# Kernel tuning notes

Hardware: AMD Instinct MI355X
Metric: run time of the kernel (lower is better)

Reference implementation:

```python
import jax, jax.numpy as jnp
import numpy as np

N_NODES = 50000
N_EDGES = 800000
D = 128


def _gcn_layer(x, src, dst, deg_inv_sqrt, W, b, n_nodes):
    # GCNConv: X' = D^{-1/2} (A + I) D^{-1/2} X W + b   (PyG default, self-loops added)
    h = x @ W  # [N, D]
    norm = deg_inv_sqrt[src] * deg_inv_sqrt[dst]  # [E+N]
    msgs = h[src] * norm[:, None]  # [E+N, D] gather + scale
    out = jax.ops.segment_sum(msgs, dst, num_segments=n_nodes)  # scatter-add
    return out + b


def setup_inputs() -> dict:
    key = jax.random.key(0)
    k1, k2, k3, k4 = jax.random.split(key, 4)
    x = jax.random.normal(k1, (N_NODES, D), dtype=jnp.float32)
    edge_index = jax.random.randint(k2, (2, N_EDGES), 0, N_NODES, dtype=jnp.int64)
    scale = 1.0 / np.sqrt(D)
    W1 = jax.random.normal(k3, (D, D), dtype=jnp.float32) * scale
    b1 = jnp.zeros((D,), dtype=jnp.float32)
    W2 = jax.random.normal(k4, (D, D), dtype=jnp.float32) * scale
    b2 = jnp.zeros((D,), dtype=jnp.float32)
    return {"x": x, "edge_index": edge_index, "W1": W1, "b1": b1, "W2": W2, "b2": b2}


def reference(x, edge_index, W1, b1, W2, b2):
    n_nodes = x.shape[0]
    # add self-loops once (same graph both layers)
    loop = jnp.arange(n_nodes, dtype=edge_index.dtype)
    src = jnp.concatenate([edge_index[0], loop])
    dst = jnp.concatenate([edge_index[1], loop])
    deg = jax.ops.segment_sum(jnp.ones_like(dst, dtype=x.dtype), dst, num_segments=n_nodes)
    deg_inv_sqrt = jnp.where(deg > 0, jax.lax.rsqrt(deg), 0.0)

    h = _gcn_layer(x, src, dst, deg_inv_sqrt, W1, b1, n_nodes)
    h = jax.nn.relu(h)
    h = _gcn_layer(h, src, dst, deg_inv_sqrt, W2, b2, n_nodes)
    h = jax.nn.relu(h)
    return h
```

## Files before the change

kernel.cpp:

```cpp
#include <hip/hip_runtime.h>

#define N_NODES 50000
#define N_EDGES 800000
#define D 128
#define NB 196
#define CHUNK 4096
#define NBKT 196
#define LHM (NBKT * NB)
#define NSB 151

typedef unsigned int uint32;
typedef unsigned short ushort;
typedef __attribute__((ext_vector_type(8))) short s8v;
typedef __attribute__((ext_vector_type(4))) float f4v;

__device__ __forceinline__ ushort f2bf(float f) {
    unsigned u = __float_as_uint(f);
    u += 0x7FFFu + ((u >> 16) & 1u);
    return (ushort)(u >> 16);
}
__device__ __forceinline__ float bf_lo(uint32 u) { return __uint_as_float(u << 16); }
__device__ __forceinline__ float bf_hi(uint32 u) { return __uint_as_float(u & 0xFFFF0000u); }

__device__ __forceinline__ int block_incl_scan(int v, int t) {
    int lane = t & 63, wv = t >> 6;
    int incl = v;
    #pragma unroll
    for (int off = 1; off < 64; off <<= 1) {
        int u = __shfl_up(incl, off, 64);
        if (lane >= off) incl += u;
    }
    __shared__ int wsums[4];
    if (lane == 63) wsums[wv] = incl;
    __syncthreads();
    int add = 0;
    if (wv > 0) add += wsums[0];
    if (wv > 1) add += wsums[1];
    if (wv > 2) add += wsums[2];
    return incl + add;
}

__global__ __launch_bounds__(256) void phaseA_kernel(const int* __restrict__ dst,
                                                     int* __restrict__ histM) {
    __shared__ int cnt[NBKT];
    int t = threadIdx.x, blk = blockIdx.x;
    if (t < NBKT) cnt[t] = 0;
    __syncthreads();
    int e0 = blk * CHUNK;
    for (int i = t; i < CHUNK; i += 256) {
        int e = e0 + i;
        if (e < N_EDGES) atomicAdd(&cnt[dst[e] >> 8], 1);
    }
    __syncthreads();
    if (t < NBKT) histM[t * NB + blk] = cnt[t];
}

__global__ __launch_bounds__(256) void scan1g(const int* __restrict__ in,
                                              int* __restrict__ out,
                                              int* __restrict__ bsum) {
    int t = threadIdx.x, blk = blockIdx.x;
    int i = blk * 256 + t;
    int v = (i < LHM) ? in[i] : 0;
    int incl = block_incl_scan(v, t);
    if (i < LHM) out[i] = incl - v;
    if (t == 255) bsum[blk] = incl;
}
__global__ __launch_bounds__(256) void scan2g(const int* __restrict__ bsum,
                                              int* __restrict__ boff) {
    int t = threadIdx.x;
    int v = (t < NSB) ? bsum[t] : 0;
    int incl = block_incl_scan(v, t);
    if (t < NSB) boff[t] = incl - v;
}
__global__ __launch_bounds__(256) void scan3g(int* __restrict__ out,
                                              const int* __restrict__ boff) {
    int i = blockIdx.x * 256 + threadIdx.x;
    if (i < LHM) out[i] += boff[blockIdx.x];
}

__global__ __launch_bounds__(256) void phaseC_kernel(const int* __restrict__ src,
                                                     const int* __restrict__ dst,
                                                     const int* __restrict__ base,
                                                     uint32* __restrict__ edgeTmp) {
    __shared__ int cur[NBKT];
    int t = threadIdx.x, blk = blockIdx.x;
    if (t < NBKT) cur[t] = base[t * NB + blk];
    __syncthreads();
    int e0 = blk * CHUNK;
    for (int i = t; i < CHUNK; i += 256) {
        int e = e0 + i;
        if (e < N_EDGES) {
            uint32 s = (uint32)src[e], d = (uint32)dst[e];
            int p = atomicAdd(&cur[d >> 8], 1);
            edgeTmp[p] = (s << 16) | d;
        }
    }
}

__global__ __launch_bounds__(256) void phaseD_kernel(const uint32* __restrict__ edgeTmp,
                                                     const int* __restrict__ base,
                                                     int* __restrict__ rowstart,
                                                     float* __restrict__ dis,
                                                     ushort* __restrict__ e16) {
    __shared__ int cnt[256];
    __shared__ int cur[256];
    int t = threadIdx.x, b = blockIdx.x;
    int beg = base[b * NB];
    int end = (b == NBKT - 1) ? N_EDGES : base[(b + 1) * NB];
    cnt[t] = 0;
    __syncthreads();
    for (int p = beg + t; p < end; p += 256)
        atomicAdd(&cnt[edgeTmp[p] & 255], 1);
    __syncthreads();
    int c = cnt[t];
    int incl = block_incl_scan(c, t);
    int excl = incl - c;
    int node = b * 256 + t;
    if (node <= N_NODES) rowstart[node] = beg + excl;
    if (node < N_NODES) dis[node] = rsqrtf((float)(c + 1));
    cur[t] = excl;
    __syncthreads();
    for (int p = beg + t; p < end; p += 256) {
        uint32 u = edgeTmp[p];
        int r = atomicAdd(&cur[u & 255], 1);
        e16[beg + r] = (ushort)(u >> 16);
    }
}

__global__ __launch_bounds__(256) void wprep_kernel(const float* __restrict__ W1,
                                                    const float* __restrict__ W2,
                                                    ushort* __restrict__ W1t,
                                                    ushort* __restrict__ W2t) {
    const float* W = blockIdx.x ? W2 : W1;
    ushort* Wt = blockIdx.x ? W2t : W1t;
    int t = threadIdx.x;
    #pragma unroll
    for (int it = 0; it < 16; it++) {
        int fid = t + it * 256;
        int k = fid >> 5;
        int n0 = (fid & 31) * 4;
        float4 w = ((const float4*)W)[fid];
        Wt[(n0 + 0) * D + k] = f2bf(w.x);
        Wt[(n0 + 1) * D + k] = f2bf(w.y);
        Wt[(n0 + 2) * D + k] = f2bf(w.z);
        Wt[(n0 + 3) * D + k] = f2bf(w.w);
    }
}

template<bool BF16IN>
__global__ __launch_bounds__(256) void gemm_mfma(const void* __restrict__ Xv,
                                                 const ushort* __restrict__ Wt,
                                                 const float* __restrict__ dis,
                                                 ushort* __restrict__ Hb) {
    __shared__ ushort Cs[128 * 136];
    int t = threadIdx.x;
    int wv = t >> 6, lane = t & 63;
    int q = lane >> 4, m = lane & 15;
    int rbase = blockIdx.x * 128 + wv * 32;
    f4v zero = {0.f, 0.f, 0.f, 0.f};
    f4v acc[2][8];
    #pragma unroll
    for (int mt = 0; mt < 2; mt++)
        #pragma unroll
        for (int n = 0; n < 8; n++) acc[mt][n] = zero;

    #pragma unroll
    for (int kt = 0; kt < 4; kt++) {
        int k0 = kt * 32 + q * 8;
        s8v a[2];
        #pragma unroll
        for (int mt = 0; mt < 2; mt++) {
            int row = rbase + mt * 16 + m;
            if (row >= N_NODES) row = N_NODES - 1;
            if (BF16IN) {
                const ushort* xp = (const ushort*)Xv + (size_t)row * D + k0;
                a[mt] = *(const s8v*)xp;
            } else {
                const float* xp = (const float*)Xv + (size_t)row * D + k0;
                float4 u0 = *(const float4*)xp;
                float4 u1 = *(const float4*)(xp + 4);
                s8v av;
                av[0] = (short)f2bf(u0.x); av[1] = (short)f2bf(u0.y);
                av[2] = (short)f2bf(u0.z); av[3] = (short)f2bf(u0.w);
                av[4] = (short)f2bf(u1.x); av[5] = (short)f2bf(u1.y);
                av[6] = (short)f2bf(u1.z); av[7] = (short)f2bf(u1.w);
                a[mt] = av;
            }
        }
        #pragma unroll
        for (int n = 0; n < 8; n++) {
            s8v b = *(const s8v*)(Wt + (size_t)(n * 16 + m) * D + k0);
            acc[0][n] = __builtin_amdgcn_mfma_f32_16x16x32_bf16(a[0], b, acc[0][n], 0, 0, 0);
            acc[1][n] = __builtin_amdgcn_mfma_f32_16x16x32_bf16(a[1], b, acc[1][n], 0, 0, 0);
        }
    }
    float disv[2][4];
    #pragma unroll
    for (int mt = 0; mt < 2; mt++)
        #pragma unroll
        for (int r = 0; r < 4; r++) {
            int row = rbase + mt * 16 + q * 4 + r;
            if (row >= N_NODES) row = N_NODES - 1;
            disv[mt][r] = dis[row];
        }
    #pragma unroll
    for (int mt = 0; mt < 2; mt++)
        #pragma unroll
        for (int n = 0; n < 8; n++)
            #pragma unroll
            for (int r = 0; r < 4; r++) {
                int row = wv * 32 + mt * 16 + q * 4 + r;
                Cs[row * 136 + n * 16 + m] = f2bf(acc[mt][n][r] * disv[mt][r]);
            }
    __syncthreads();
    int gbase = blockIdx.x * 128;
    #pragma unroll
    for (int it = 0; it < 8; it++) {
        int cid = t + it * 256;
        int row = cid >> 4, off = (cid & 15) * 8;
        int grow = gbase + row;
        if (grow < N_NODES) {
            s8v v = *(const s8v*)(Cs + row * 136 + off);
            *(s8v*)(Hb + (size_t)grow * D + off) = v;
        }
    }
}

__device__ __forceinline__ void acc8(float* a, uint4 v) {
    a[0] += bf_lo(v.x); a[1] += bf_hi(v.x);
    a[2] += bf_lo(v.y); a[3] += bf_hi(v.y);
    a[4] += bf_lo(v.z); a[5] += bf_hi(v.z);
    a[6] += bf_lo(v.w); a[7] += bf_hi(v.w);
}

template<bool BF16OUT>
__global__ __launch_bounds__(256) void aggr_kernel(const uint4* __restrict__ Hb4,
                                                   const float* __restrict__ dis,
                                                   const int* __restrict__ rowstart,
                                                   const ushort* __restrict__ e16,
                                                   const float* __restrict__ bias,
                                                   void* __restrict__ Hout) {
    int t = threadIdx.x;
    int li = t & 15;
    int n = blockIdx.x * 16 + (t >> 4);
    float dn = dis[n];
    float a[8];
    {
        uint4 sv = Hb4[(size_t)n * 16 + li];
        a[0] = bf_lo(sv.x); a[1] = bf_hi(sv.x);
        a[2] = bf_lo(sv.y); a[3] = bf_hi(sv.y);
        a[4] = bf_lo(sv.z); a[5] = bf_hi(sv.z);
        a[6] = bf_lo(sv.w); a[7] = bf_hi(sv.w);
    }
    int beg = rowstart[n], end = rowstart[n + 1];
    int p = beg;
    for (; p + 3 < end; p += 4) {
        int s0 = e16[p + 0], s1 = e16[p + 1], s2 = e16[p + 2], s3 = e16[p + 3];
        uint4 v0 = Hb4[(size_t)s0 * 16 + li];
        uint4 v1 = Hb4[(size_t)s1 * 16 + li];
        uint4 v2 = Hb4[(size_t)s2 * 16 + li];
        uint4 v3 = Hb4[(size_t)s3 * 16 + li];
        acc8(a, v0); acc8(a, v1); acc8(a, v2); acc8(a, v3);
    }
    for (; p < end; p++) {
        uint4 v0 = Hb4[(size_t)e16[p] * 16 + li];
        acc8(a, v0);
    }
    const float4* b4 = (const float4*)bias;
    float4 bb0 = b4[li * 2], bb1 = b4[li * 2 + 1];
    float r0 = fmaxf(fmaf(dn, a[0], bb0.x), 0.f);
    float r1 = fmaxf(fmaf(dn, a[1], bb0.y), 0.f);
    float r2 = fmaxf(fmaf(dn, a[2], bb0.z), 0.f);
    float r3 = fmaxf(fmaf(dn, a[3], bb0.w), 0.f);
    float r4 = fmaxf(fmaf(dn, a[4], bb1.x), 0.f);
    float r5 = fmaxf(fmaf(dn, a[5], bb1.y), 0.f);
    float r6 = fmaxf(fmaf(dn, a[6], bb1.z), 0.f);
    float r7 = fmaxf(fmaf(dn, a[7], bb1.w), 0.f);
    if (BF16OUT) {
        uint4 o;
        o.x = (uint32)f2bf(r0) | ((uint32)f2bf(r1) << 16);
        o.y = (uint32)f2bf(r2) | ((uint32)f2bf(r3) << 16);
        o.z = (uint32)f2bf(r4) | ((uint32)f2bf(r5) << 16);
        o.w = (uint32)f2bf(r6) | ((uint32)f2bf(r7) << 16);
        ((uint4*)Hout)[(size_t)n * 16 + li] = o;
    } else {
        float4* H4 = (float4*)Hout;
        float4 o0; o0.x = r0; o0.y = r1; o0.z = r2; o0.w = r3;
        float4 o1; o1.x = r4; o1.y = r5; o1.z = r6; o1.w = r7;
        H4[(size_t)n * 32 + li * 2]     = o0;
        H4[(size_t)n * 32 + li * 2 + 1] = o1;
    }
}

extern "C" void kernel_launch(void* const* d_in, const int* in_sizes, int n_in,
                              void* d_out, int out_size, void* d_ws, size_t ws_size,
                              hipStream_t stream) {
    const float* x  = (const float*)d_in[0];
    const int*   ei = (const int*)d_in[1];
    const float* W1 = (const float*)d_in[2];
    const float* b1 = (const float*)d_in[3];
    const float* W2 = (const float*)d_in[4];
    const float* b2 = (const float*)d_in[5];
    float* out = (float*)d_out;

    char* ws = (char*)d_ws;
    size_t off = 0;
    auto alloc = [&](size_t bytes) -> void* {
        void* p = ws + off;
        off += (bytes + 255) & ~(size_t)255;
        return p;
    };
    int*    histM    = (int*)alloc((size_t)LHM * 4);
    int*    base     = (int*)alloc((size_t)LHM * 4);
    int*    bsum     = (int*)alloc(256 * 4);
    int*    boff     = (int*)alloc(256 * 4);
    int*    rowstart = (int*)alloc((size_t)(N_NODES + 1) * 4);
    float*  dis      = (float*)alloc((size_t)N_NODES * 4);
    uint32* edgeTmp  = (uint32*)alloc((size_t)N_EDGES * 4);
    ushort* e16      = (ushort*)alloc((size_t)N_EDGES * 2);
    ushort* Hb       = (ushort*)alloc((size_t)N_NODES * D * 2);
    ushort* HO1      = (ushort*)alloc((size_t)N_NODES * D * 2);
    ushort* W1t      = (ushort*)alloc((size_t)D * D * 2);
    ushort* W2t      = (ushort*)alloc((size_t)D * D * 2);

    const int* src = ei;
    const int* dst = ei + N_EDGES;

    wprep_kernel<<<2, 256, 0, stream>>>(W1, W2, W1t, W2t);
    phaseA_kernel<<<NB, 256, 0, stream>>>(dst, histM);
    scan1g<<<NSB, 256, 0, stream>>>(histM, base, bsum);
    scan2g<<<1, 256, 0, stream>>>(bsum, boff);
    scan3g<<<NSB, 256, 0, stream>>>(base, boff);
    phaseC_kernel<<<NB, 256, 0, stream>>>(src, dst, base, edgeTmp);
    phaseD_kernel<<<NBKT, 256, 0, stream>>>(edgeTmp, base, rowstart, dis, e16);

    gemm_mfma<false><<<(N_NODES + 127) / 128, 256, 0, stream>>>(x, W1t, dis, Hb);
    aggr_kernel<true><<<N_NODES / 16, 256, 0, stream>>>((const uint4*)Hb, dis, rowstart,
                                                        e16, b1, HO1);
    gemm_mfma<true><<<(N_NODES + 127) / 128, 256, 0, stream>>>(HO1, W2t, dis, Hb);
    aggr_kernel<false><<<N_NODES / 16, 256, 0, stream>>>((const uint4*)Hb, dis, rowstart,
                                                         e16, b2, out);
}
```

Measured before the change: 216.4 us.

## Fuse weight prep into histogram, merge scan passes, refine buckets, unroll aggregation by 8

Folds the weight transpose/bf16 conversion into extra blocks of the histogram kernel and merges the second and third scan kernels into one that recomputes block offsets by reduction, cutting two launches. Bucket size shrinks from 256 to 128 nodes and edge chunks halve, doubling block counts for the CSR build phases. The aggregation kernel gains an 8-way unrolled gather loop to raise memory-level parallelism. The larger histogram and the per-block prefix reduction add some redundant work.

```diff
diff --git a/kernel.cpp b/kernel.cpp
--- a/kernel.cpp
+++ b/kernel.cpp
@@ -3,11 +3,11 @@
 #define N_NODES 50000
 #define N_EDGES 800000
 #define D 128
-#define NB 196
-#define CHUNK 4096
-#define NBKT 196
+#define NB 392
+#define CHUNK 2048
+#define NBKT 391
 #define LHM (NBKT * NB)
-#define NSB 151
+#define NSB ((LHM + 255) / 256)
 
 typedef unsigned int uint32;
 typedef unsigned short ushort;
@@ -41,18 +41,39 @@
 }
 
 __global__ __launch_bounds__(256) void phaseA_kernel(const int* __restrict__ dst,
-                                                     int* __restrict__ histM) {
+                                                     int* __restrict__ histM,
+                                                     const float* __restrict__ W1,
+                                                     const float* __restrict__ W2,
+                                                     ushort* __restrict__ W1t,
+                                                     ushort* __restrict__ W2t) {
     __shared__ int cnt[NBKT];
     int t = threadIdx.x, blk = blockIdx.x;
-    if (t < NBKT) cnt[t] = 0;
+    if (blk >= NB) {
+        const float* W = (blk - NB) ? W2 : W1;
+        ushort* Wt = (blk - NB) ? W2t : W1t;
+        #pragma unroll
+        for (int it = 0; it < 16; it++) {
+            int fid = t + it * 256;
+            int k = fid >> 5;
+            int n0 = (fid & 31) * 4;
+            float4 w = ((const float4*)W)[fid];
+            Wt[(n0 + 0) * D + k] = f2bf(w.x);
+            Wt[(n0 + 1) * D + k] = f2bf(w.y);
+            Wt[(n0 + 2) * D + k] = f2bf(w.z);
+            Wt[(n0 + 3) * D + k] = f2bf(w.w);
+        }
+        return;
+    }
+    for (int i = t; i < NBKT; i += 256) cnt[i] = 0;
     __syncthreads();
     int e0 = blk * CHUNK;
     for (int i = t; i < CHUNK; i += 256) {
         int e = e0 + i;
-        if (e < N_EDGES) atomicAdd(&cnt[dst[e] >> 8], 1);
-    }
-    __syncthreads();
-    if (t < NBKT) histM[t * NB + blk] = cnt[t];
+        if (e < N_EDGES) atomicAdd(&cnt[dst[e] >> 7], 1);
+    }
+    __syncthreads();
+    for (int i = t; i < NBKT; i += 256)
+        histM[i * NB + blk] = cnt[i];
 }
 
 __global__ __launch_bounds__(256) void scan1g(const int* __restrict__ in,
@@ -65,17 +86,21 @@
     if (i < LHM) out[i] = incl - v;
     if (t == 255) bsum[blk] = incl;
 }
-__global__ __launch_bounds__(256) void scan2g(const int* __restrict__ bsum,
-                                              int* __restrict__ boff) {
-    int t = threadIdx.x;
-    int v = (t < NSB) ? bsum[t] : 0;
-    int incl = block_incl_scan(v, t);
-    if (t < NSB) boff[t] = incl - v;
-}
-__global__ __launch_bounds__(256) void scan3g(int* __restrict__ out,
-                                              const int* __restrict__ boff) {
-    int i = blockIdx.x * 256 + threadIdx.x;
-    if (i < LHM) out[i] += boff[blockIdx.x];
+
+__global__ __launch_bounds__(256) void scan23g(int* __restrict__ out,
+                                               const int* __restrict__ bsum) {
+    int t = threadIdx.x, blk = blockIdx.x;
+    int local = 0;
+    for (int i = t; i < blk; i += 256) local += bsum[i];
+    int lane = t & 63, wv = t >> 6;
+    #pragma unroll
+    for (int off = 32; off > 0; off >>= 1) local += __shfl_down(local, off, 64);
+    __shared__ int ws[4];
+    if (lane == 0) ws[wv] = local;
+    __syncthreads();
+    int boff = ws[0] + ws[1] + ws[2] + ws[3];
+    int i = blk * 256 + t;
+    if (i < LHM) out[i] += boff;
 }
 
 __global__ __launch_bounds__(256) void phaseC_kernel(const int* __restrict__ src,
@@ -84,14 +109,14 @@
                                                      uint32* __restrict__ edgeTmp) {
     __shared__ int cur[NBKT];
     int t = threadIdx.x, blk = blockIdx.x;
-    if (t < NBKT) cur[t] = base[t * NB + blk];
+    for (int i = t; i < NBKT; i += 256) cur[i] = base[i * NB + blk];
     __syncthreads();
     int e0 = blk * CHUNK;
     for (int i = t; i < CHUNK; i += 256) {
         int e = e0 + i;
         if (e < N_EDGES) {
             uint32 s = (uint32)src[e], d = (uint32)dst[e];
-            int p = atomicAdd(&cur[d >> 8], 1);
+            int p = atomicAdd(&cur[d >> 7], 1);
             edgeTmp[p] = (s << 16) | d;
         }
     }
@@ -102,48 +127,31 @@
                                                      int* __restrict__ rowstart,
                                                      float* __restrict__ dis,
                                                      ushort* __restrict__ e16) {
-    __shared__ int cnt[256];
-    __shared__ int cur[256];
+    __shared__ int cnt[128];
+    __shared__ int cur[128];
     int t = threadIdx.x, b = blockIdx.x;
     int beg = base[b * NB];
     int end = (b == NBKT - 1) ? N_EDGES : base[(b + 1) * NB];
-    cnt[t] = 0;
+    if (t < 128) cnt[t] = 0;
     __syncthreads();
     for (int p = beg + t; p < end; p += 256)
-        atomicAdd(&cnt[edgeTmp[p] & 255], 1);
-    __syncthreads();
-    int c = cnt[t];
+        atomicAdd(&cnt[edgeTmp[p] & 127], 1);
+    __syncthreads();
+    int c = (t < 128) ? cnt[t] : 0;
     int incl = block_incl_scan(c, t);
     int excl = incl - c;
-    int node = b * 256 + t;
-    if (node <= N_NODES) rowstart[node] = beg + excl;
-    if (node < N_NODES) dis[node] = rsqrtf((float)(c + 1));
-    cur[t] = excl;
+    int node = b * 128 + t;
+    if (t <= 128 && node <= N_NODES) {
+        if (t < 128) rowstart[node] = beg + excl;
+    }
+    if (t == 128 && node <= N_NODES) rowstart[node] = end;
+    if (t < 128 && node < N_NODES) dis[node] = rsqrtf((float)(c + 1));
+    if (t < 128) cur[t] = excl;
     __syncthreads();
     for (int p = beg + t; p < end; p += 256) {
         uint32 u = edgeTmp[p];
-        int r = atomicAdd(&cur[u & 255], 1);
+        int r = atomicAdd(&cur[u & 127], 1);
         e16[beg + r] = (ushort)(u >> 16);
-    }
-}
-
-__global__ __launch_bounds__(256) void wprep_kernel(const float* __restrict__ W1,
-                                                    const float* __restrict__ W2,
-                                                    ushort* __restrict__ W1t,
-                                                    ushort* __restrict__ W2t) {
-    const float* W = blockIdx.x ? W2 : W1;
-    ushort* Wt = blockIdx.x ? W2t : W1t;
-    int t = threadIdx.x;
-    #pragma unroll
-    for (int it = 0; it < 16; it++) {
-        int fid = t + it * 256;
-        int k = fid >> 5;
-        int n0 = (fid & 31) * 4;
-        float4 w = ((const float4*)W)[fid];
-        Wt[(n0 + 0) * D + k] = f2bf(w.x);
-        Wt[(n0 + 1) * D + k] = f2bf(w.y);
-        Wt[(n0 + 2) * D + k] = f2bf(w.z);
-        Wt[(n0 + 3) * D + k] = f2bf(w.w);
     }
 }
 
@@ -254,6 +262,16 @@
     }
     int beg = rowstart[n], end = rowstart[n + 1];
     int p = beg;
+    for (; p + 7 < end; p += 8) {
+        int s[8];
+        #pragma unroll
+        for (int j = 0; j < 8; j++) s[j] = e16[p + j];
+        uint4 v[8];
+        #pragma unroll
+        for (int j = 0; j < 8; j++) v[j] = Hb4[(size_t)s[j] * 16 + li];
+        #pragma unroll
+        for (int j = 0; j < 8; j++) acc8(a, v[j]);
+    }
     for (; p + 3 < end; p += 4) {
         int s0 = e16[p + 0], s1 = e16[p + 1], s2 = e16[p + 2], s3 = e16[p + 3];
         uint4 v0 = Hb4[(size_t)s0 * 16 + li];
@@ -312,8 +330,7 @@
     };
     int*    histM    = (int*)alloc((size_t)LHM * 4);
     int*    base     = (int*)alloc((size_t)LHM * 4);
-    int*    bsum     = (int*)alloc(256 * 4);
-    int*    boff     = (int*)alloc(256 * 4);
+    int*    bsum     = (int*)alloc((size_t)NSB * 4);
     int*    rowstart = (int*)alloc((size_t)(N_NODES + 1) * 4);
     float*  dis      = (float*)alloc((size_t)N_NODES * 4);
     uint32* edgeTmp  = (uint32*)alloc((size_t)N_EDGES * 4);
@@ -326,11 +343,9 @@
     const int* src = ei;
     const int* dst = ei + N_EDGES;
 
-    wprep_kernel<<<2, 256, 0, stream>>>(W1, W2, W1t, W2t);
-    phaseA_kernel<<<NB, 256, 0, stream>>>(dst, histM);
+    phaseA_kernel<<<NB + 2, 256, 0, stream>>>(dst, histM, W1, W2, W1t, W2t);
     scan1g<<<NSB, 256, 0, stream>>>(histM, base, bsum);
-    scan2g<<<1, 256, 0, stream>>>(bsum, boff);
-    scan3g<<<NSB, 256, 0, stream>>>(base, boff);
+    scan23g<<<NSB, 256, 0, stream>>>(base, bsum);
     phaseC_kernel<<<NB, 256, 0, stream>>>(src, dst, base, edgeTmp);
     phaseD_kernel<<<NBKT, 256, 0, stream>>>(edgeTmp, base, rowstart, dis, e16);
 
```

Result: faster. 209.5 us (-3.2%).
